# Kernel tuning notes

Measured on AMD Instinct MI355X. Metric: run time of the kernel, lower is better.

The kernel has to match this reference:

```python
import jax, jax.numpy as jnp
import numpy as np

B, F, W, H, D = 128, 1024, 32, 64, 64  # batch, n_features, window_size, hidden_state, output_dim


def setup_inputs() -> dict:
    key = jax.random.key(0)
    ks = jax.random.split(key, 8)
    sd = 0.05
    return {
        "x": jax.random.normal(ks[0], (B, F, W), jnp.float32),
        # dense_state: Dense(output_dim) on concat([cell, hidden]) -> [2H, D]
        "W_state": jax.random.normal(ks[1], (2 * H, D), jnp.float32) * sd,
        "b_state": jnp.zeros((D,), jnp.float32),
        # dense: Dense(output_dim, use_bias=False) on input last dim W -> [W, D]
        "W_in": jax.random.normal(ks[2], (W, D), jnp.float32) * sd,
        # Dense(1) scoring layer (shared; original re-creates it each call)
        "w_attn": jax.random.normal(ks[3], (D, 1), jnp.float32) * sd,
        "b_attn": jnp.zeros((1,), jnp.float32),
        # Keras LSTMCell params, gate order i, f, g(c~), o
        "Wx": jax.random.normal(ks[4], (F, 4 * H), jnp.float32) * sd,
        "Wh": jax.random.normal(ks[5], (H, 4 * H), jnp.float32) * sd,
        "b_lstm": jnp.zeros((4 * H,), jnp.float32),
    }


def _forward(x, W_state, b_state, W_in, w_attn, b_attn, Wx, Wh, b_lstm):
    b, f, w = x.shape
    h_dim = Wh.shape[0]
    # dense(input) is loop-invariant: [B, F, D]
    dense_in = jnp.einsum('bfw,wd->bfd', x, W_in)
    xs = jnp.moveaxis(x, 2, 0)  # [W, B, F]: per-timestep slices input[:, :, i]
    h0 = jnp.zeros((b, h_dim), x.dtype)
    c0 = jnp.zeros((b, h_dim), x.dtype)

    def step(carry, x_t):
        h, c = carry
        # original unpacks `s, h = state` with state=[h,c], so it concats [cell, hidden]
        attn_in = jnp.concatenate([c, h], axis=1)             # [B, 2H]
        z = jnp.tanh(attn_in @ W_state + b_state)[:, None, :] + dense_in  # [B, F, D]
        presoft = z @ w_attn + b_attn                         # [B, F, 1]
        # faithful: softmax over last (size-1) axis -> all ones
        alpha = jax.nn.softmax(presoft, axis=-1)
        x_tilde = alpha[..., 0] * x_t                         # [B, F]
        gates = x_tilde @ Wx + h @ Wh + b_lstm                # [B, 4H]
        i_g, f_g, g_g, o_g = jnp.split(gates, 4, axis=1)
        c_new = jax.nn.sigmoid(f_g) * c + jax.nn.sigmoid(i_g) * jnp.tanh(g_g)
        h_new = jax.nn.sigmoid(o_g) * jnp.tanh(c_new)
        # original appends state[1] == CELL state (due to the s,h swap)
        return (h_new, c_new), c_new

    _, outs = jax.lax.scan(step, (h0, c0), xs)                # [W, B, H]
    return jnp.transpose(outs, (1, 0, 2))                     # [B, W, H]


def reference(x, W_state, b_state, W_in, w_attn, b_attn, Wx, Wh, b_lstm):
    return _forward(x, W_state, b_state, W_in, w_attn, b_attn, Wx, Wh, b_lstm)
```

## Files before the change

### kernel.cpp

```cpp
#include <hip/hip_runtime.h>
#include <math.h>

#define B_   128
#define F_   1024
#define W_   32
#define H_   64
#define K4H  256
#define M_   (B_ * W_)
#define K2_  (2 * F_)

typedef __attribute__((ext_vector_type(8))) short  short8;
typedef __attribute__((ext_vector_type(4))) float  f32x4;

__device__ __forceinline__ unsigned bf16_rne(float v) {
  unsigned u = __float_as_uint(v);
  return (u + 0x7FFFu + ((u >> 16) & 1u)) >> 16;
}
__device__ __forceinline__ unsigned pack_hilo(float v) {
  unsigned hi = bf16_rne(v);
  float    hf = __uint_as_float(hi << 16);
  unsigned lo = bf16_rne(v - hf);
  return hi | (lo << 16);
}

__global__ __launch_bounds__(256) void conv_w(const float* __restrict__ Wx,
                                              unsigned* __restrict__ B2) {
  __shared__ unsigned T[256][17];
  const int tid = threadIdx.x;
  const int f0  = blockIdx.x * 16;
#pragma unroll
  for (int i = 0; i < 4; ++i) {
    int l = tid + i * 256;
    int n0 = (l & 63) * 4;
    int fl = l >> 6;
    float4 v = *(const float4*)&Wx[(size_t)(f0 + fl) * K4H + n0];
    T[n0 + 0][fl] = pack_hilo(v.x);
    T[n0 + 1][fl] = pack_hilo(v.y);
    T[n0 + 2][fl] = pack_hilo(v.z);
    T[n0 + 3][fl] = pack_hilo(v.w);
  }
  __syncthreads();
#pragma unroll
  for (int i = 0; i < 4; ++i) {
    int l  = tid + i * 256;
    int c4 = (l & 3) * 4;
    int n  = l >> 2;
    uint4 o;
    o.x = T[n][c4 + 0]; o.y = T[n][c4 + 1]; o.z = T[n][c4 + 2]; o.w = T[n][c4 + 3];
    *(uint4*)&B2[(size_t)n * (K2_ / 2) + f0 + c4] = o;
  }
}

template <int S>
__global__ __launch_bounds__(256, 1) void gemm_mfma(
    const float* __restrict__ x,
    const unsigned* __restrict__ B2,
    float* __restrict__ Gp) {
  constexpr int NIT = 32 / S;
  __shared__ unsigned lA[128 * 36];
  __shared__ unsigned lB[128 * 36];
  const int tid   = threadIdx.x;
  const int mtile = blockIdx.x;
  const int ntile = blockIdx.y;
  const int s     = blockIdx.z;
  const int wv = tid >> 6, lane = tid & 63;
  const int wm = wv & 1, wn = wv >> 1;
  const int lm = lane & 15, q = lane >> 4;

  f32x4 acc[4][4];
#pragma unroll
  for (int a = 0; a < 4; ++a)
#pragma unroll
    for (int bb = 0; bb < 4; ++bb) acc[a][bb] = (f32x4){0.f, 0.f, 0.f, 0.f};

  const int b0 = mtile * 4;
  float4 ax[4];
  uint4  bxr[4];

  auto prefetch = [&](int iter) {
    const int f0 = (s * NIT + iter) * 32;
#pragma unroll
    for (int i = 0; i < 4; ++i) {
      int l  = tid + i * 256;
      int t0 = (l & 7) * 4;
      int fl = (l >> 3) & 31;
      int bl = l >> 8;
      ax[i] = *(const float4*)&x[(((size_t)(b0 + bl)) * F_ + (f0 + fl)) * W_ + t0];
    }
#pragma unroll
    for (int i = 0; i < 4; ++i) {
      int l   = tid + i * 256;
      int c16 = l & 7;
      int nl  = l >> 3;
      bxr[i] = *(const uint4*)&B2[(size_t)(ntile * 128 + nl) * (K2_ / 2) + f0 + c16 * 4];
    }
  };

  prefetch(0);
  const int jx = (tid >> 3) & 3;
  for (int iter = 0; iter < NIT; ++iter) {
    __syncthreads();
#pragma unroll
    for (int i = 0; i < 4; ++i) {
      int l  = tid + i * 256;
      int t0 = (l & 7) * 4;
      int fl = (l >> 3) & 31;
      int bl = l >> 8;
      int m0 = bl * 32 + t0;
      float vals[4] = {ax[i].x, ax[i].y, ax[i].z, ax[i].w};
#pragma unroll
      for (int j = 0; j < 4; ++j) {
        int jj = j ^ jx;
        lA[(m0 + jj) * 36 + fl] = pack_hilo(vals[jj]);
      }
    }
#pragma unroll
    for (int i = 0; i < 4; ++i) {
      int l   = tid + i * 256;
      int c16 = l & 7;
      int nl  = l >> 3;
      *(uint4*)&lB[nl * 36 + c16 * 4] = bxr[i];
    }
    __syncthreads();
    if (iter + 1 < NIT) prefetch(iter + 1);
#pragma unroll
    for (int step = 0; step < 2; ++step) {
      short8 aF[4], bF[4];
#pragma unroll
      for (int mt = 0; mt < 4; ++mt) {
        int row = wm * 64 + mt * 16 + lm;
        aF[mt] = *(const short8*)&lA[row * 36 + step * 16 + q * 4];
      }
#pragma unroll
      for (int nt = 0; nt < 4; ++nt) {
        int row = wn * 64 + nt * 16 + lm;
        bF[nt] = *(const short8*)&lB[row * 36 + step * 16 + q * 4];
      }
#pragma unroll
      for (int mt = 0; mt < 4; ++mt)
#pragma unroll
        for (int nt = 0; nt < 4; ++nt)
          acc[mt][nt] = __builtin_amdgcn_mfma_f32_16x16x32_bf16(
              aF[mt], bF[nt], acc[mt][nt], 0, 0, 0);
    }
  }
  float* Gs = Gp + (size_t)s * ((size_t)M_ * K4H);
#pragma unroll
  for (int mt = 0; mt < 4; ++mt)
#pragma unroll
    for (int nt = 0; nt < 4; ++nt)
#pragma unroll
      for (int r = 0; r < 4; ++r) {
        int m = mtile * 128 + wm * 64 + mt * 16 + q * 4 + r;
        int n = ntile * 128 + wn * 64 + nt * 16 + lm;
        Gs[(size_t)m * K4H + n] = acc[mt][nt][r];
      }
}

__device__ __forceinline__ float bcastlane(float v, int l) {
  return __uint_as_float(__builtin_amdgcn_readlane(__float_as_uint(v), l));
}
__device__ __forceinline__ float sigm(float v)   { return 1.f / (1.f + __expf(-v)); }
__device__ __forceinline__ float tanh_f(float v) { return 1.f - 2.f / (__expf(2.f * v) + 1.f); }

template <int S>
__global__ __launch_bounds__(256, 1) void lstm_seq(
    const float* __restrict__ Gp, const float* __restrict__ Wh,
    const float* __restrict__ bl, float* __restrict__ out) {
  __shared__ float sG[32 * 260];
  __shared__ float sact[2][4][64];
  const int b = blockIdx.x, tid = threadIdx.x;
  const int w = tid >> 6, u = tid & 63;
  const int k = w * 64 + u;

  float wc[64];
#pragma unroll
  for (int j = 0; j < 64; ++j) wc[j] = Wh[j * K4H + k];
  const float bk = bl[k];

  const float4* G4 = (const float4*)Gp + (size_t)b * 32 * (K4H / 4);
  const size_t  s4 = (size_t)M_ * K4H / 4;
#pragma unroll
  for (int i = 0; i < 8; ++i) {
    int idx = tid + i * 256;
    int t = idx >> 6, c = idx & 63;
    float4 v = G4[(size_t)t * (K4H / 4) + c];
#pragma unroll
    for (int ss = 1; ss < S; ++ss) {
      float4 p = G4[(size_t)ss * s4 + (size_t)t * (K4H / 4) + c];
      v.x += p.x; v.y += p.y; v.z += p.z; v.w += p.w;
    }
    *(float4*)&sG[t * 260 + c * 4] = v;
  }
  __syncthreads();

  float h = 0.f, c = 0.f;
  float gc = sG[k];
#pragma unroll 1
  for (int t = 0; t < W_; ++t) {
    float gn = (t + 1 < W_) ? sG[(t + 1) * 260 + k] : 0.f;
    float g0 = gc + bk, g1 = 0.f, g2 = 0.f, g3 = 0.f;
#pragma unroll
    for (int j = 0; j < 64; j += 4) {
      g0 = fmaf(bcastlane(h, j),     wc[j],     g0);
      g1 = fmaf(bcastlane(h, j + 1), wc[j + 1], g1);
      g2 = fmaf(bcastlane(h, j + 2), wc[j + 2], g2);
      g3 = fmaf(bcastlane(h, j + 3), wc[j + 3], g3);
    }
    float g = (g0 + g1) + (g2 + g3);
    float act = (w == 2) ? tanh_f(g) : sigm(g);
    sact[t & 1][w][u] = act;
    __syncthreads();
    float si = sact[t & 1][0][u];
    float sf = sact[t & 1][1][u];
    float tg = sact[t & 1][2][u];
    float so = sact[t & 1][3][u];
    c = fmaf(sf, c, si * tg);
    h = so * tanh_f(c);
    if (w == 0) sG[t * 260 + u] = c;
    gc = gn;
  }
  __syncthreads();

#pragma unroll
  for (int i = 0; i < 2; ++i) {
    int id = tid * 2 + i;
    int t  = id >> 4, u4 = (id & 15) * 4;
    float4 o = *(const float4*)&sG[t * 260 + u4];
    *(float4*)&out[((size_t)b * W_ + t) * H_ + u4] = o;
  }
}

extern "C" void kernel_launch(void* const* d_in, const int* in_sizes, int n_in,
                              void* d_out, int out_size, void* d_ws, size_t ws_size,
                              hipStream_t stream) {
  const float* x      = (const float*)d_in[0];
  const float* Wx     = (const float*)d_in[6];
  const float* Wh     = (const float*)d_in[7];
  const float* b_lstm = (const float*)d_in[8];
  float* out = (float*)d_out;

  const size_t gbytes = (size_t)M_ * K4H * sizeof(float);

  if (ws_size >= 4 * gbytes + (1u << 20)) {
    float*    Gp = (float*)d_ws;
    unsigned* B2 = (unsigned*)((char*)d_ws + 4 * gbytes);
    conv_w      <<<dim3(64),       dim3(256), 0, stream>>>(Wx, B2);
    gemm_mfma<4><<<dim3(32, 2, 4), dim3(256), 0, stream>>>(x, B2, Gp);
    lstm_seq<4> <<<dim3(B_),       dim3(256), 0, stream>>>(Gp, Wh, b_lstm, out);
  } else if (ws_size >= 2 * gbytes + (1u << 20)) {
    float*    Gp = (float*)d_ws;
    unsigned* B2 = (unsigned*)((char*)d_ws + 2 * gbytes);
    conv_w      <<<dim3(64),       dim3(256), 0, stream>>>(Wx, B2);
    gemm_mfma<2><<<dim3(32, 2, 2), dim3(256), 0, stream>>>(x, B2, Gp);
    lstm_seq<2> <<<dim3(B_),       dim3(256), 0, stream>>>(Gp, Wh, b_lstm, out);
  } else {
    float*    Gp = (float*)d_ws;
    unsigned* B2 = (unsigned*)((char*)d_ws + gbytes);
    conv_w      <<<dim3(64),       dim3(256), 0, stream>>>(Wx, B2);
    gemm_mfma<1><<<dim3(32, 2, 1), dim3(256), 0, stream>>>(x, B2, Gp);
    lstm_seq<1> <<<dim3(B_),       dim3(256), 0, stream>>>(Gp, Wh, b_lstm, out);
  }
}
```

Measured before the change: 124.6 us.

## Fuse weight conversion, GEMM and LSTM into one persistent kernel with grid barriers

Replaces the three separate launches (weight packing, split-K MFMA GEMM, LSTM recurrence) with a single 256-block persistent kernel. Phases are separated by software grid barriers built on per-block flags with alternating magic values. The first x tile is prefetched before the weight-conversion phase so global loads overlap it. This removes the inter-kernel launch and drain gaps. In exchange it relies on all 256 blocks being co-resident and adds spin-wait barrier overhead. Flags are never reset, so correctness on the first call depends on the workspace not already holding a magic value.

```diff
diff --git a/kernel.cpp b/kernel.cpp
--- a/kernel.cpp
+++ b/kernel.cpp
@@ -8,6 +8,11 @@
 #define K4H  256
 #define M_   (B_ * W_)
 #define K2_  (2 * F_)
+#define S_   4
+#define NIT_ 8
+
+#define MAGIC_A 0x9E3779B1u
+#define MAGIC_B 0x85EBCA77u
 
 typedef __attribute__((ext_vector_type(8))) short  short8;
 typedef __attribute__((ext_vector_type(4))) float  f32x4;
@@ -21,6 +26,233 @@
   float    hf = __uint_as_float(hi << 16);
   unsigned lo = bf16_rne(v - hf);
   return hi | (lo << 16);
+}
+__device__ __forceinline__ float bcastlane(float v, int l) {
+  return __uint_as_float(__builtin_amdgcn_readlane(__float_as_uint(v), l));
+}
+__device__ __forceinline__ float sigm(float v)   { return 1.f / (1.f + __expf(-v)); }
+__device__ __forceinline__ float tanh_f(float v) { return 1.f - 2.f / (__expf(2.f * v) + 1.f); }
+
+__device__ __forceinline__ void gridbar(unsigned* flags, int bid, int tid,
+                                        unsigned magic) {
+  __syncthreads();
+  __threadfence();
+  if (tid == 0)
+    __hip_atomic_store(&flags[bid], magic, __ATOMIC_RELEASE,
+                       __HIP_MEMORY_SCOPE_AGENT);
+  while (__hip_atomic_load(&flags[tid], __ATOMIC_ACQUIRE,
+                           __HIP_MEMORY_SCOPE_AGENT) != magic)
+    __builtin_amdgcn_s_sleep(1);
+  __threadfence();
+  __syncthreads();
+}
+
+__global__ __launch_bounds__(256, 1) void mega(
+    const float* __restrict__ x,
+    const float* __restrict__ Wx,
+    const float* __restrict__ Wh,
+    const float* __restrict__ bl,
+    unsigned* __restrict__ B2,
+    float* __restrict__ Gp,
+    unsigned* __restrict__ flags,
+    float* __restrict__ out) {
+  __shared__ __align__(16) unsigned smem[9216];
+  const int bid = blockIdx.x;
+  const int tid = threadIdx.x;
+  const int wv = tid >> 6, lane = tid & 63;
+  const int wm = wv & 1, wn = wv >> 1;
+  const int lm = lane & 15, q = lane >> 4;
+
+  const int mtile = bid & 31, ntile = (bid >> 5) & 1, s = bid >> 6;
+  const int b0 = mtile * 4;
+
+  float4 ax[4];
+  uint4  bxr[4];
+  auto pre_x = [&](int iter) {
+    const int f0 = (s * NIT_ + iter) * 32;
+#pragma unroll
+    for (int i = 0; i < 4; ++i) {
+      int l  = tid + i * 256;
+      int t0 = (l & 7) * 4;
+      int fl = (l >> 3) & 31;
+      int blb = l >> 8;
+      ax[i] = *(const float4*)&x[(((size_t)(b0 + blb)) * F_ + (f0 + fl)) * W_ + t0];
+    }
+  };
+  auto pre_b = [&](int iter) {
+    const int f0 = (s * NIT_ + iter) * 32;
+#pragma unroll
+    for (int i = 0; i < 4; ++i) {
+      int l   = tid + i * 256;
+      int c16 = l & 7;
+      int nl  = l >> 3;
+      bxr[i] = *(const uint4*)&B2[(size_t)(ntile * 128 + nl) * (K2_ / 2) + f0 + c16 * 4];
+    }
+  };
+
+  pre_x(0);
+
+  if (bid < 64) {
+    unsigned (*T)[17] = (unsigned (*)[17])smem;
+    const int f0c = bid * 16;
+#pragma unroll
+    for (int i = 0; i < 4; ++i) {
+      int l  = tid + i * 256;
+      int n0 = (l & 63) * 4;
+      int fl = l >> 6;
+      float4 v = *(const float4*)&Wx[(size_t)(f0c + fl) * K4H + n0];
+      T[n0 + 0][fl] = pack_hilo(v.x);
+      T[n0 + 1][fl] = pack_hilo(v.y);
+      T[n0 + 2][fl] = pack_hilo(v.z);
+      T[n0 + 3][fl] = pack_hilo(v.w);
+    }
+    __syncthreads();
+#pragma unroll
+    for (int i = 0; i < 4; ++i) {
+      int l  = tid + i * 256;
+      int c4 = (l & 3) * 4;
+      int n  = l >> 2;
+      uint4 o;
+      o.x = T[n][c4 + 0]; o.y = T[n][c4 + 1]; o.z = T[n][c4 + 2]; o.w = T[n][c4 + 3];
+      *(uint4*)&B2[(size_t)n * (K2_ / 2) + f0c + c4] = o;
+    }
+  }
+  gridbar(flags, bid, tid, MAGIC_A);
+
+  {
+    unsigned* lA = smem;
+    unsigned* lB = smem + 128 * 36;
+    f32x4 acc[4][4];
+#pragma unroll
+    for (int a = 0; a < 4; ++a)
+#pragma unroll
+      for (int bb = 0; bb < 4; ++bb) acc[a][bb] = (f32x4){0.f, 0.f, 0.f, 0.f};
+
+    pre_b(0);
+    const int jx = (tid >> 3) & 3;
+    for (int iter = 0; iter < NIT_; ++iter) {
+      __syncthreads();
+#pragma unroll
+      for (int i = 0; i < 4; ++i) {
+        int l  = tid + i * 256;
+        int t0 = (l & 7) * 4;
+        int fl = (l >> 3) & 31;
+        int blb = l >> 8;
+        int m0 = blb * 32 + t0;
+        float vals[4] = {ax[i].x, ax[i].y, ax[i].z, ax[i].w};
+#pragma unroll
+        for (int j = 0; j < 4; ++j) {
+          int jj = j ^ jx;
+          lA[(m0 + jj) * 36 + fl] = pack_hilo(vals[jj]);
+        }
+      }
+#pragma unroll
+      for (int i = 0; i < 4; ++i) {
+        int l   = tid + i * 256;
+        int c16 = l & 7;
+        int nl  = l >> 3;
+        *(uint4*)&lB[nl * 36 + c16 * 4] = bxr[i];
+      }
+      __syncthreads();
+      if (iter + 1 < NIT_) { pre_x(iter + 1); pre_b(iter + 1); }
+#pragma unroll
+      for (int step = 0; step < 2; ++step) {
+        short8 aF[4], bF[4];
+#pragma unroll
+        for (int mt = 0; mt < 4; ++mt) {
+          int row = wm * 64 + mt * 16 + lm;
+          aF[mt] = *(const short8*)&lA[row * 36 + step * 16 + q * 4];
+        }
+#pragma unroll
+        for (int nt = 0; nt < 4; ++nt) {
+          int row = wn * 64 + nt * 16 + lm;
+          bF[nt] = *(const short8*)&lB[row * 36 + step * 16 + q * 4];
+        }
+#pragma unroll
+        for (int mt = 0; mt < 4; ++mt)
+#pragma unroll
+          for (int nt = 0; nt < 4; ++nt)
+            acc[mt][nt] = __builtin_amdgcn_mfma_f32_16x16x32_bf16(
+                aF[mt], bF[nt], acc[mt][nt], 0, 0, 0);
+      }
+    }
+    float* Gs = Gp + (size_t)s * ((size_t)M_ * K4H);
+#pragma unroll
+    for (int mt = 0; mt < 4; ++mt)
+#pragma unroll
+      for (int nt = 0; nt < 4; ++nt)
+#pragma unroll
+        for (int r = 0; r < 4; ++r) {
+          int m = mtile * 128 + wm * 64 + mt * 16 + q * 4 + r;
+          int n = ntile * 128 + wn * 64 + nt * 16 + lm;
+          Gs[(size_t)m * K4H + n] = acc[mt][nt][r];
+        }
+  }
+  gridbar(flags, bid, tid, MAGIC_B);
+
+  if (bid < B_) {
+    float* sm = (float*)smem;
+    float* sG = sm;
+    float (*sact)[4][64] = (float (*)[4][64])(sm + 32 * 260);
+    const int b = bid, w = wv, u = lane;
+    const int k = w * 64 + u;
+
+    float wc[64];
+#pragma unroll
+    for (int j = 0; j < 64; ++j) wc[j] = Wh[j * K4H + k];
+    const float bk = bl[k];
+
+    const float4* G4 = (const float4*)Gp + (size_t)b * 32 * (K4H / 4);
+    const size_t  s4 = (size_t)M_ * K4H / 4;
+#pragma unroll
+    for (int i = 0; i < 8; ++i) {
+      int idx = tid + i * 256;
+      int t = idx >> 6, c = idx & 63;
+      float4 v = G4[(size_t)t * (K4H / 4) + c];
+#pragma unroll
+      for (int ss = 1; ss < S_; ++ss) {
+        float4 p = G4[(size_t)ss * s4 + (size_t)t * (K4H / 4) + c];
+        v.x += p.x; v.y += p.y; v.z += p.z; v.w += p.w;
+      }
+      *(float4*)&sG[t * 260 + c * 4] = v;
+    }
+    __syncthreads();
+
+    float h = 0.f, c = 0.f;
+    float gc = sG[k];
+#pragma unroll 1
+    for (int t = 0; t < W_; ++t) {
+      float gn = (t + 1 < W_) ? sG[(t + 1) * 260 + k] : 0.f;
+      float g0 = gc + bk, g1 = 0.f, g2 = 0.f, g3 = 0.f;
+#pragma unroll
+      for (int j = 0; j < 64; j += 4) {
+        g0 = fmaf(bcastlane(h, j),     wc[j],     g0);
+        g1 = fmaf(bcastlane(h, j + 1), wc[j + 1], g1);
+        g2 = fmaf(bcastlane(h, j + 2), wc[j + 2], g2);
+        g3 = fmaf(bcastlane(h, j + 3), wc[j + 3], g3);
+      }
+      float g = (g0 + g1) + (g2 + g3);
+      float act = (w == 2) ? tanh_f(g) : sigm(g);
+      sact[t & 1][w][u] = act;
+      __syncthreads();
+      float si = sact[t & 1][0][u];
+      float sf = sact[t & 1][1][u];
+      float tg = sact[t & 1][2][u];
+      float so = sact[t & 1][3][u];
+      c = fmaf(sf, c, si * tg);
+      h = so * tanh_f(c);
+      if (w == 0) sG[t * 260 + u] = c;
+      gc = gn;
+    }
+    __syncthreads();
+#pragma unroll
+    for (int i = 0; i < 2; ++i) {
+      int id = tid * 2 + i;
+      int t  = id >> 4, u4 = (id & 15) * 4;
+      float4 o = *(const float4*)&sG[t * 260 + u4];
+      *(float4*)&out[((size_t)b * W_ + t) * H_ + u4] = o;
+    }
+  }
 }
 
 __global__ __launch_bounds__(256) void conv_w(const float* __restrict__ Wx,
@@ -53,8 +285,7 @@
 
 template <int S>
 __global__ __launch_bounds__(256, 1) void gemm_mfma(
-    const float* __restrict__ x,
-    const unsigned* __restrict__ B2,
+    const float* __restrict__ x, const unsigned* __restrict__ B2,
     float* __restrict__ Gp) {
   constexpr int NIT = 32 / S;
   __shared__ unsigned lA[128 * 36];
@@ -157,12 +388,6 @@
       }
 }
 
-__device__ __forceinline__ float bcastlane(float v, int l) {
-  return __uint_as_float(__builtin_amdgcn_readlane(__float_as_uint(v), l));
-}
-__device__ __forceinline__ float sigm(float v)   { return 1.f / (1.f + __expf(-v)); }
-__device__ __forceinline__ float tanh_f(float v) { return 1.f - 2.f / (__expf(2.f * v) + 1.f); }
-
 template <int S>
 __global__ __launch_bounds__(256, 1) void lstm_seq(
     const float* __restrict__ Gp, const float* __restrict__ Wh,
@@ -221,7 +446,6 @@
     gc = gn;
   }
   __syncthreads();
-
 #pragma unroll
   for (int i = 0; i < 2; ++i) {
     int id = tid * 2 + i;
@@ -242,12 +466,12 @@
 
   const size_t gbytes = (size_t)M_ * K4H * sizeof(float);
 
-  if (ws_size >= 4 * gbytes + (1u << 20)) {
-    float*    Gp = (float*)d_ws;
-    unsigned* B2 = (unsigned*)((char*)d_ws + 4 * gbytes);
-    conv_w      <<<dim3(64),       dim3(256), 0, stream>>>(Wx, B2);
-    gemm_mfma<4><<<dim3(32, 2, 4), dim3(256), 0, stream>>>(x, B2, Gp);
-    lstm_seq<4> <<<dim3(B_),       dim3(256), 0, stream>>>(Gp, Wh, b_lstm, out);
+  if (ws_size >= 4 * gbytes + (2u << 20)) {
+    float*    Gp    = (float*)d_ws;
+    unsigned* B2    = (unsigned*)((char*)d_ws + 4 * gbytes);
+    unsigned* flags = (unsigned*)((char*)d_ws + 4 * gbytes + (1u << 20));
+    mega<<<dim3(256), dim3(256), 0, stream>>>(x, Wx, Wh, b_lstm, B2, Gp,
+                                              flags, out);
   } else if (ws_size >= 2 * gbytes + (1u << 20)) {
     float*    Gp = (float*)d_ws;
     unsigned* B2 = (unsigned*)((char*)d_ws + 2 * gbytes);
```

Result: slower. 252.6 us (+102.7%).
